# Performance work log

Measured on AMD Instinct MI355X. Metric: run time of the kernel, lower is better.

## Reference

```python
import jax, jax.numpy as jnp
import numpy as np

B, N = 256, 512
DIM_GRAPH = 256
DIM_DESC = 256
RANK = 64


def setup_inputs() -> dict:
    key = jax.random.key(0)
    ks = jax.random.split(key, 6)
    tokns_k = jax.random.normal(ks[0], (B, DIM_DESC), dtype=jnp.float32)
    H_pad = jax.random.normal(ks[1], (B, N, DIM_GRAPH), dtype=jnp.float32)
    mask = jax.random.randint(ks[2], (B, N), 0, 2).astype(bool)
    mask = mask.at[:, 0].set(True)  # ensure at least one valid node per graph
    # Linear weights, torch convention: y = x @ W.T
    Wq = jax.random.normal(ks[3], (RANK, DIM_DESC), dtype=jnp.float32) / np.sqrt(DIM_DESC)
    Wk = jax.random.normal(ks[4], (RANK, DIM_GRAPH), dtype=jnp.float32) / np.sqrt(DIM_GRAPH)
    Wv = jax.random.normal(ks[5], (DIM_DESC, DIM_GRAPH), dtype=jnp.float32) / np.sqrt(DIM_GRAPH)
    log_scale = jnp.zeros((1,), dtype=jnp.float32)
    return {"tokns_k": tokns_k, "H_pad": H_pad, "mask": mask,
            "Wq": Wq, "Wk": Wk, "Wv": Wv, "log_scale": log_scale}


def reference(tokns_k, H_pad, mask, Wq, Wk, Wv, log_scale):
    q = tokns_k @ Wq.T                                  # [B, r]
    k = jnp.einsum('bnd,rd->bnr', H_pad, Wk)            # [B, N, r]
    scale = jnp.maximum(jnp.exp(log_scale), 0.1)        # clamp(min=0.1)
    scores = jnp.einsum('br,bnr->bn', q, k) / scale     # [B, N]
    neg_inf = jnp.float32(-jnp.inf)
    scores = jnp.where(mask, scores, neg_inf)
    alpha = jax.nn.softmax(scores, axis=-1)             # [B, N]
    v = jnp.einsum('bnd,ed->bne', H_pad, Wv)            # [B, N, dim_desc]
    ctx_k = jnp.einsum('bn,bne->be', alpha, v)          # [B, dim_desc]
    return (alpha, ctx_k)
```

## Files before the change

### kernel.cpp

```cpp
#include <hip/hip_runtime.h>

constexpr int Bc = 256;
constexpr int Nc = 512;
constexpr int Dc = 256;
constexpr int Rc = 64;
constexpr int SPLIT = 8;
constexpr int ROWS = Nc / SPLIT;

constexpr size_t WS_P = 0;
constexpr size_t WS_L = WS_P + (size_t)Bc * Dc;
constexpr size_t WS_H = WS_L + (size_t)Bc * SPLIT;
constexpr size_t WS_FLOATS = WS_H + (size_t)Bc * SPLIT * Dc;

__global__ __launch_bounds__(256) void k0_precompute_p(
    const float* __restrict__ tokns_k, const float* __restrict__ Wq,
    const float* __restrict__ Wk, float* __restrict__ ws)
{
    const int b = blockIdx.x;
    const int t = threadIdx.x;
    const int wave = t >> 6, lane = t & 63, g = lane >> 4, l16 = lane & 15;

    __shared__ float q_s[Rc];

    #pragma unroll
    for (int step = 0; step < 4; ++step) {
        const int r = wave * 16 + step * 4 + g;
        float acc = 0.0f;
        #pragma unroll
        for (int j = 0; j < 4; ++j) {
            const float4 tk = *(const float4*)(tokns_k + b * Dc + l16 * 4 + j * 64);
            const float4 wq = *(const float4*)(Wq + r * Dc + l16 * 4 + j * 64);
            acc += tk.x * wq.x + tk.y * wq.y + tk.z * wq.z + tk.w * wq.w;
        }
        #pragma unroll
        for (int off = 1; off < 16; off <<= 1) acc += __shfl_xor(acc, off);
        if (l16 == 0) q_s[r] = acc;
    }
    __syncthreads();

    float acc = 0.0f;
    #pragma unroll 8
    for (int r = 0; r < Rc; ++r) acc += q_s[r] * Wk[r * Dc + t];
    ws[WS_P + (size_t)b * Dc + t] = acc;
}

__global__ __launch_bounds__(256) void k1_stream(
    const float* __restrict__ H_pad, const int* __restrict__ mask,
    const float* __restrict__ log_scale, float* __restrict__ ws,
    float* __restrict__ out)
{
    const int s = blockIdx.x;
    const int b = blockIdx.y;
    const int t = threadIdx.x;
    const int wave = t >> 6, lane = t & 63, g = lane >> 4, l16 = lane & 15;
    const int n0 = s * ROWS;

    __shared__ __align__(16) float hm[16][Dc];
    __shared__ float l_s[16];
    __shared__ float scores_s[ROWS];
    __shared__ int   mask_s[ROWS];

    if (t < ROWS) mask_s[t] = mask[b * Nc + n0 + t];

    const float inv_scale = 1.0f / fmaxf(__expf(log_scale[0]), 0.1f);

    const float* __restrict__ pb = ws + WS_P + (size_t)b * Dc;
    float4 p4[4];
    #pragma unroll
    for (int j = 0; j < 4; ++j) p4[j] = *(const float4*)(pb + l16 * 4 + j * 64);
    __syncthreads();

    const float* __restrict__ Hb = H_pad + ((size_t)b * Nc + n0) * Dc;
    float  l_acc = 0.0f;
    float4 h4[4];
    #pragma unroll
    for (int j = 0; j < 4; ++j) h4[j] = make_float4(0.f, 0.f, 0.f, 0.f);

    #pragma unroll
    for (int step = 0; step < 4; ++step) {
        const int nr = step * 16 + wave * 4 + g;
        const float* __restrict__ row = Hb + nr * Dc + l16 * 4;
        float4 x[4];
        #pragma unroll
        for (int j = 0; j < 4; ++j) x[j] = *(const float4*)(row + j * 64);

        float s0 = x[0].x * p4[0].x + x[0].y * p4[0].y + x[0].z * p4[0].z + x[0].w * p4[0].w;
        float s1 = x[1].x * p4[1].x + x[1].y * p4[1].y + x[1].z * p4[1].z + x[1].w * p4[1].w;
        float s2 = x[2].x * p4[2].x + x[2].y * p4[2].y + x[2].z * p4[2].z + x[2].w * p4[2].w;
        float s3 = x[3].x * p4[3].x + x[3].y * p4[3].y + x[3].z * p4[3].z + x[3].w * p4[3].w;
        float sc = (s0 + s1) + (s2 + s3);
        #pragma unroll
        for (int off = 1; off < 16; off <<= 1) sc += __shfl_xor(sc, off);
        sc *= inv_scale;
        if (mask_s[nr] == 0) sc = -1e30f;
        if (l16 == 0) scores_s[nr] = sc;

        const float pn = __expf(sc);
        l_acc += pn;
        #pragma unroll
        for (int j = 0; j < 4; ++j) {
            h4[j].x = fmaf(pn, x[j].x, h4[j].x);
            h4[j].y = fmaf(pn, x[j].y, h4[j].y);
            h4[j].z = fmaf(pn, x[j].z, h4[j].z);
            h4[j].w = fmaf(pn, x[j].w, h4[j].w);
        }
    }

    const int team = wave * 4 + g;
    #pragma unroll
    for (int j = 0; j < 4; ++j) *(float4*)(&hm[team][l16 * 4 + j * 64]) = h4[j];
    if (l16 == 0) l_s[team] = l_acc;
    __syncthreads();

    if (t < ROWS) out[b * Nc + n0 + t] = scores_s[t];
    float hsum = 0.0f;
    #pragma unroll
    for (int p = 0; p < 16; ++p) hsum += hm[p][t];
    ws[WS_H + ((size_t)b * SPLIT + s) * Dc + t] = hsum;
    if (t == 0) {
        float L = 0.0f;
        #pragma unroll
        for (int p = 0; p < 16; ++p) L += l_s[p];
        ws[WS_L + (size_t)b * SPLIT + s] = L;
    }
}

__global__ __launch_bounds__(256) void k2_merge(
    const float* __restrict__ Wv, const float* __restrict__ ws,
    float* __restrict__ out)
{
    const int b = blockIdx.x;
    const int t = threadIdx.x;
    const int wave = t >> 6, lane = t & 63, g = lane >> 4, l16 = lane & 15;

    __shared__ __align__(16) float hbar[Dc];

    float L = 0.0f;
    #pragma unroll
    for (int s = 0; s < SPLIT; ++s) L += ws[WS_L + (size_t)b * SPLIT + s];
    const float invL = 1.0f / L;

    float hacc = 0.0f;
    #pragma unroll
    for (int s = 0; s < SPLIT; ++s) hacc += ws[WS_H + ((size_t)b * SPLIT + s) * Dc + t];
    hbar[t] = hacc * invL;

    #pragma unroll
    for (int i = 0; i < Nc / 256; ++i) {
        const int idx = b * Nc + i * 256 + t;
        out[idx] = __expf(out[idx]) * invL;
    }
    __syncthreads();

    float4 hb4[4];
    #pragma unroll
    for (int j = 0; j < 4; ++j) hb4[j] = *(const float4*)(hbar + l16 * 4 + j * 64);
    float* __restrict__ ctx_out = out + (size_t)Bc * Nc + b * Dc;
    #pragma unroll
    for (int step = 0; step < 16; ++step) {
        const int e = step * 16 + wave * 4 + g;
        float acc = 0.0f;
        #pragma unroll
        for (int j = 0; j < 4; ++j) {
            const float4 wv = *(const float4*)(Wv + e * Dc + l16 * 4 + j * 64);
            acc += wv.x * hb4[j].x + wv.y * hb4[j].y + wv.z * hb4[j].z + wv.w * hb4[j].w;
        }
        #pragma unroll
        for (int off = 1; off < 16; off <<= 1) acc += __shfl_xor(acc, off);
        if (l16 == 0) ctx_out[e] = acc;
    }
}

constexpr int FNT = 512;
constexpr int FNW = FNT / 64;
constexpr int FNPW = Nc / FNW;

__global__ __launch_bounds__(FNT) void fba_fallback(
    const float* __restrict__ tokns_k, const float* __restrict__ H_pad,
    const int* __restrict__ mask, const float* __restrict__ Wq,
    const float* __restrict__ Wk, const float* __restrict__ Wv,
    const float* __restrict__ log_scale, float* __restrict__ out)
{
    const int b = blockIdx.x, t = threadIdx.x;
    const int wave = t >> 6, lane = t & 63;

    __shared__ __align__(16) float q_s[Rc];
    __shared__ __align__(16) float p_s[Dc];
    __shared__ __align__(16) float scores_s[Nc];
    __shared__ __align__(16) float hmerge[FNW][Dc];
    __shared__ float l_s[FNW];
    __shared__ __align__(16) float hbar[Dc];
    __shared__ int mask_s[Nc];

    const float inv_scale = 1.0f / fmaxf(__expf(log_scale[0]), 0.1f);

    const float4 tok4 = *(const float4*)(tokns_k + b * Dc + lane * 4);
    #pragma unroll
    for (int i = 0; i < Rc / FNW; ++i) {
        const int r = wave * (Rc / FNW) + i;
        const float4 w4 = *(const float4*)(Wq + r * Dc + lane * 4);
        float s = w4.x * tok4.x + w4.y * tok4.y + w4.z * tok4.z + w4.w * tok4.w;
        #pragma unroll
        for (int off = 32; off >= 1; off >>= 1) s += __shfl_xor(s, off);
        if (lane == 0) q_s[r] = s;
    }
    mask_s[t] = mask[b * Nc + t];
    mask_s[t + FNT] = mask[b * Nc + t + FNT];
    __syncthreads();

    if (t < Dc) {
        float acc = 0.0f;
        #pragma unroll 8
        for (int r = 0; r < Rc; ++r) acc += q_s[r] * Wk[r * Dc + t];
        p_s[t] = acc;
    }
    __syncthreads();

    const float4 p4 = *(const float4*)(p_s + lane * 4);
    const float* Hb = H_pad + (size_t)b * Nc * Dc;
    float l_acc = 0.0f;
    float4 h4 = make_float4(0.f, 0.f, 0.f, 0.f);

    for (int i = 0; i < FNPW; ++i) {
        const int n = wave * FNPW + i;
        const float4 x4 = *(const float4*)(Hb + n * Dc + lane * 4);
        float s = x4.x * p4.x + x4.y * p4.y + x4.z * p4.z + x4.w * p4.w;
        #pragma unroll
        for (int off = 32; off >= 1; off >>= 1) s += __shfl_xor(s, off);
        s *= inv_scale;
        if (mask_s[n] == 0) s = -1e30f;
        if (lane == 0) scores_s[n] = s;
        const float pn = __expf(s);
        l_acc += pn;
        h4.x = fmaf(pn, x4.x, h4.x); h4.y = fmaf(pn, x4.y, h4.y);
        h4.z = fmaf(pn, x4.z, h4.z); h4.w = fmaf(pn, x4.w, h4.w);
    }

    if (lane == 0) l_s[wave] = l_acc;
    *(float4*)(&hmerge[wave][lane * 4]) = h4;
    __syncthreads();

    float L = 0.0f;
    #pragma unroll
    for (int w = 0; w < FNW; ++w) L += l_s[w];
    const float invL = 1.0f / L;

    if (t < Dc) {
        float acc = 0.0f;
        #pragma unroll
        for (int w = 0; w < FNW; ++w) acc += hmerge[w][t];
        hbar[t] = acc * invL;
    }
    out[b * Nc + t] = __expf(scores_s[t]) * invL;
    out[b * Nc + t + FNT] = __expf(scores_s[t + FNT]) * invL;
    __syncthreads();

    const float4 hb4 = *(const float4*)(hbar + lane * 4);
    float* ctx_out = out + (size_t)Bc * Nc + b * Dc;
    #pragma unroll
    for (int i = 0; i < Dc / FNW; ++i) {
        const int e = wave * (Dc / FNW) + i;
        const float4 w4 = *(const float4*)(Wv + e * Dc + lane * 4);
        float s = w4.x * hb4.x + w4.y * hb4.y + w4.z * hb4.z + w4.w * hb4.w;
        #pragma unroll
        for (int off = 32; off >= 1; off >>= 1) s += __shfl_xor(s, off);
        if (lane == 0) ctx_out[e] = s;
    }
}

extern "C" void kernel_launch(void* const* d_in, const int* in_sizes, int n_in,
                              void* d_out, int out_size, void* d_ws, size_t ws_size,
                              hipStream_t stream) {
    const float* tokns_k   = (const float*)d_in[0];
    const float* H_pad     = (const float*)d_in[1];
    const int*   mask      = (const int*)d_in[2];
    const float* Wq        = (const float*)d_in[3];
    const float* Wk        = (const float*)d_in[4];
    const float* Wv        = (const float*)d_in[5];
    const float* log_scale = (const float*)d_in[6];
    float* out = (float*)d_out;

    if (ws_size >= WS_FLOATS * sizeof(float)) {
        float* ws = (float*)d_ws;
        k0_precompute_p<<<Bc, 256, 0, stream>>>(tokns_k, Wq, Wk, ws);
        dim3 grid1(SPLIT, Bc);
        k1_stream<<<grid1, 256, 0, stream>>>(H_pad, mask, log_scale, ws, out);
        k2_merge<<<Bc, 256, 0, stream>>>(Wv, ws, out);
    } else {
        fba_fallback<<<Bc, FNT, 0, stream>>>(tokns_k, H_pad, mask, Wq, Wk, Wv,
                                             log_scale, out);
    }
}
```

Measured before the change: 223.3 us.

## Split score and weighted-sum phases with different thread-to-row mappings in stream kernel

The streaming kernel now computes scores with 8 threads per row, which shortens the shuffle reduction, and stores the exponentials in shared memory. A second pass re-reads each row, this time with 16 threads per row, to accumulate the p-weighted sum of H. The normalizer L is now reduced from the shared exponentials with a wave shuffle. H rows are loaded twice (the second read is likely served from cache), and the block synchronizes once per group of 32 rows, adding barrier and reload cost in exchange for less shuffle work.

```diff
diff --git a/kernel.cpp b/kernel.cpp
--- a/kernel.cpp
+++ b/kernel.cpp
@@ -6,6 +6,7 @@
 constexpr int Rc = 64;
 constexpr int SPLIT = 8;
 constexpr int ROWS = Nc / SPLIT;
+constexpr int GROUP = 32;
 
 constexpr size_t WS_P = 0;
 constexpr size_t WS_L = WS_P + (size_t)Bc * Dc;
@@ -52,11 +53,15 @@
     const int s = blockIdx.x;
     const int b = blockIdx.y;
     const int t = threadIdx.x;
-    const int wave = t >> 6, lane = t & 63, g = lane >> 4, l16 = lane & 15;
     const int n0 = s * ROWS;
 
+    const int rowA = t >> 3;
+    const int e    = t & 7;
+    const int tau  = t >> 4;
+    const int l16  = t & 15;
+
     __shared__ __align__(16) float hm[16][Dc];
-    __shared__ float l_s[16];
+    __shared__ float pn_s[ROWS];
     __shared__ float scores_s[ROWS];
     __shared__ int   mask_s[ROWS];
 
@@ -65,64 +70,74 @@
     const float inv_scale = 1.0f / fmaxf(__expf(log_scale[0]), 0.1f);
 
     const float* __restrict__ pb = ws + WS_P + (size_t)b * Dc;
-    float4 p4[4];
-    #pragma unroll
-    for (int j = 0; j < 4; ++j) p4[j] = *(const float4*)(pb + l16 * 4 + j * 64);
-    __syncthreads();
+    float4 pA[8];
+    #pragma unroll
+    for (int k = 0; k < 8; ++k) pA[k] = *(const float4*)(pb + (e + 8 * k) * 4);
 
     const float* __restrict__ Hb = H_pad + ((size_t)b * Nc + n0) * Dc;
-    float  l_acc = 0.0f;
+
     float4 h4[4];
     #pragma unroll
     for (int j = 0; j < 4; ++j) h4[j] = make_float4(0.f, 0.f, 0.f, 0.f);
 
-    #pragma unroll
-    for (int step = 0; step < 4; ++step) {
-        const int nr = step * 16 + wave * 4 + g;
-        const float* __restrict__ row = Hb + nr * Dc + l16 * 4;
-        float4 x[4];
-        #pragma unroll
-        for (int j = 0; j < 4; ++j) x[j] = *(const float4*)(row + j * 64);
-
-        float s0 = x[0].x * p4[0].x + x[0].y * p4[0].y + x[0].z * p4[0].z + x[0].w * p4[0].w;
-        float s1 = x[1].x * p4[1].x + x[1].y * p4[1].y + x[1].z * p4[1].z + x[1].w * p4[1].w;
-        float s2 = x[2].x * p4[2].x + x[2].y * p4[2].y + x[2].z * p4[2].z + x[2].w * p4[2].w;
-        float s3 = x[3].x * p4[3].x + x[3].y * p4[3].y + x[3].z * p4[3].z + x[3].w * p4[3].w;
-        float sc = (s0 + s1) + (s2 + s3);
-        #pragma unroll
-        for (int off = 1; off < 16; off <<= 1) sc += __shfl_xor(sc, off);
-        sc *= inv_scale;
-        if (mask_s[nr] == 0) sc = -1e30f;
-        if (l16 == 0) scores_s[nr] = sc;
-
-        const float pn = __expf(sc);
-        l_acc += pn;
-        #pragma unroll
-        for (int j = 0; j < 4; ++j) {
-            h4[j].x = fmaf(pn, x[j].x, h4[j].x);
-            h4[j].y = fmaf(pn, x[j].y, h4[j].y);
-            h4[j].z = fmaf(pn, x[j].z, h4[j].z);
-            h4[j].w = fmaf(pn, x[j].w, h4[j].w);
+    __syncthreads();
+
+    #pragma unroll
+    for (int g = 0; g < ROWS / GROUP; ++g) {
+        {
+            const int n = g * GROUP + rowA;
+            const float* __restrict__ row = Hb + n * Dc;
+            float4 x[8];
+            #pragma unroll
+            for (int k = 0; k < 8; ++k) x[k] = *(const float4*)(row + (e + 8 * k) * 4);
+            float acc = 0.0f;
+            #pragma unroll
+            for (int k = 0; k < 8; ++k)
+                acc += x[k].x * pA[k].x + x[k].y * pA[k].y
+                     + x[k].z * pA[k].z + x[k].w * pA[k].w;
+            acc += __shfl_xor(acc, 1);
+            acc += __shfl_xor(acc, 2);
+            acc += __shfl_xor(acc, 4);
+            acc *= inv_scale;
+            if (mask_s[n] == 0) acc = -1e30f;
+            if (e == 0) {
+                scores_s[n] = acc;
+                pn_s[n] = __expf(acc);
+            }
         }
-    }
-
-    const int team = wave * 4 + g;
-    #pragma unroll
-    for (int j = 0; j < 4; ++j) *(float4*)(&hm[team][l16 * 4 + j * 64]) = h4[j];
-    if (l16 == 0) l_s[team] = l_acc;
+        __syncthreads();
+
+        #pragma unroll
+        for (int r = 0; r < 2; ++r) {
+            const int n = g * GROUP + tau * 2 + r;
+            const float pn = pn_s[n];
+            const float* __restrict__ row = Hb + n * Dc;
+            #pragma unroll
+            for (int j = 0; j < 4; ++j) {
+                const float4 x = *(const float4*)(row + (l16 + 16 * j) * 4);
+                h4[j].x = fmaf(pn, x.x, h4[j].x);
+                h4[j].y = fmaf(pn, x.y, h4[j].y);
+                h4[j].z = fmaf(pn, x.z, h4[j].z);
+                h4[j].w = fmaf(pn, x.w, h4[j].w);
+            }
+        }
+    }
+
+    #pragma unroll
+    for (int j = 0; j < 4; ++j) *(float4*)(&hm[tau][(l16 + 16 * j) * 4]) = h4[j];
     __syncthreads();
 
     if (t < ROWS) out[b * Nc + n0 + t] = scores_s[t];
+    if (t < ROWS) {
+        float L = pn_s[t];
+        #pragma unroll
+        for (int off = 32; off >= 1; off >>= 1) L += __shfl_xor(L, off);
+        if (t == 0) ws[WS_L + (size_t)b * SPLIT + s] = L;
+    }
     float hsum = 0.0f;
     #pragma unroll
     for (int p = 0; p < 16; ++p) hsum += hm[p][t];
     ws[WS_H + ((size_t)b * SPLIT + s) * Dc + t] = hsum;
-    if (t == 0) {
-        float L = 0.0f;
-        #pragma unroll
-        for (int p = 0; p < 16; ++p) L += l_s[p];
-        ws[WS_L + (size_t)b * SPLIT + s] = L;
-    }
 }
 
 __global__ __launch_bounds__(256) void k2_merge(
```

Measured after the change: 227.5 us. About the same (+1.9%).
